# Kernel tuning notes

Measured on AMD Instinct MI355X. Metric: run time of the kernel, lower is better.

The kernel has to match this reference:

```python
import jax, jax.numpy as jnp
import numpy as np

# __init__ constants of RMSELoss(early, gap, late)
EARLY = 1
GAP = 0.5
LATE = 2


def setup_inputs() -> dict:
    key = jax.random.key(0)
    k1, k2 = jax.random.split(key)
    N = 16777216  # rows; column dim is 1 since forward indexes inputs[r, 0]
    inputs = jax.random.normal(k1, (N, 1), dtype=jnp.float32)
    targets = jax.random.normal(k2, (N, 1), dtype=jnp.float32)
    return {"inputs": inputs, "targets": targets}


def reference(inputs, targets):
    # train=True path of RMSELoss.forward, fully vectorized.
    d = targets - inputs  # [N, 1]
    # per-row weight: 2+early if d>=gap, 2+late if d<0, else 0 (d**0 == 1,
    # including 0**0 == 1, matching torch.pow semantics).
    early_term = d ** (2 + EARLY)  # integer_pow handles negative bases exactly
    late_term = d ** (2 + LATE)
    v = jnp.where(d >= GAP, early_term,
                  jnp.where(d < 0, late_term, jnp.ones_like(d)))
    return jnp.mean(v) ** 0.5
```

## Files before the change

### kernel.cpp

```cpp
#include <hip/hip_runtime.h>
#include <math.h>


__device__ __forceinline__ float vfun(float d) {
    float d2 = d * d;
    float e  = d2 * d;
    float l  = d2 * d2;
    return d >= 0.5f ? e : (d < 0.0f ? l : 1.0f);
}

__global__ __launch_bounds__(256) void rmse_partial(
        const float4* __restrict__ x4,
        const float4* __restrict__ t4,
        const float*  __restrict__ x,
        const float*  __restrict__ t,
        float* __restrict__ sum_ws,
        int n4, int n) {
    int idx    = blockIdx.x * blockDim.x + threadIdx.x;
    int stride = gridDim.x * blockDim.x;

    float acc = 0.0f;
    for (int i = idx; i < n4; i += stride) {
        float4 a = x4[i];
        float4 b = t4[i];
        acc += vfun(b.x - a.x);
        acc += vfun(b.y - a.y);
        acc += vfun(b.z - a.z);
        acc += vfun(b.w - a.w);
    }
    if (idx == 0) {
        for (int i = n4 * 4; i < n; ++i) acc += vfun(t[i] - x[i]);
    }

    #pragma unroll
    for (int off = 32; off > 0; off >>= 1)
        acc += __shfl_down(acc, off, 64);

    __shared__ float smem[4];
    int lane = threadIdx.x & 63;
    int wave = threadIdx.x >> 6;
    if (lane == 0) smem[wave] = acc;
    __syncthreads();
    if (threadIdx.x == 0) {
        float s = smem[0] + smem[1] + smem[2] + smem[3];
        atomicAdd(sum_ws, s);
    }
}

__global__ void rmse_final(const float* __restrict__ sum_ws,
                           float* __restrict__ out, float inv_n) {
    out[0] = sqrtf(sum_ws[0] * inv_n);
}

extern "C" void kernel_launch(void* const* d_in, const int* in_sizes, int n_in,
                              void* d_out, int out_size, void* d_ws, size_t ws_size,
                              hipStream_t stream) {
    const float* x = (const float*)d_in[0];
    const float* t = (const float*)d_in[1];
    float* out = (float*)d_out;
    float* ws  = (float*)d_ws;

    int n  = in_sizes[0];
    int n4 = n / 4;

    hipMemsetAsync(ws, 0, sizeof(float), stream);

    int grid = 2048;
    rmse_partial<<<grid, 256, 0, stream>>>(
        (const float4*)x, (const float4*)t, x, t, ws, n4, n);

    rmse_final<<<1, 1, 0, stream>>>(ws, out, 1.0f / (float)n);
}
```

Before: 161.9 us.

## Unroll loads 4x, replace atomics and memset with per-block partials reduction

The main loop now issues four float4 loads per input before computing, which raises memory-level parallelism in this bandwidth-bound reduction. The global atomicAdd and the hipMemsetAsync are removed: each block writes its partial sum to the workspace, and a 256-thread final kernel reduces the 2048 partials. This drops one launch and avoids serialised atomics, at the cost of more live registers and a larger final kernel.

```diff
diff --git a/kernel.cpp b/kernel.cpp
--- a/kernel.cpp
+++ b/kernel.cpp
@@ -1,6 +1,10 @@
 #include <hip/hip_runtime.h>
 #include <math.h>
 
+
+#define BLOCK 256
+#define GRID  2048
+#define NWAVE (BLOCK / 64)
 
 __device__ __forceinline__ float vfun(float d) {
     float d2 = d * d;
@@ -9,47 +13,82 @@
     return d >= 0.5f ? e : (d < 0.0f ? l : 1.0f);
 }
 
-__global__ __launch_bounds__(256) void rmse_partial(
+__device__ __forceinline__ float vfun4(float4 a, float4 b) {
+    return vfun(b.x - a.x) + vfun(b.y - a.y) + vfun(b.z - a.z) + vfun(b.w - a.w);
+}
+
+__global__ __launch_bounds__(BLOCK) void rmse_partial(
         const float4* __restrict__ x4,
         const float4* __restrict__ t4,
         const float*  __restrict__ x,
         const float*  __restrict__ t,
-        float* __restrict__ sum_ws,
+        float* __restrict__ block_sums,
         int n4, int n) {
     int idx    = blockIdx.x * blockDim.x + threadIdx.x;
     int stride = gridDim.x * blockDim.x;
 
     float acc = 0.0f;
-    for (int i = idx; i < n4; i += stride) {
-        float4 a = x4[i];
-        float4 b = t4[i];
-        acc += vfun(b.x - a.x);
-        acc += vfun(b.y - a.y);
-        acc += vfun(b.z - a.z);
-        acc += vfun(b.w - a.w);
+    int i = idx;
+
+    for (; i + 3 * stride < n4; i += 4 * stride) {
+        float4 a0 = x4[i];
+        float4 a1 = x4[i + stride];
+        float4 a2 = x4[i + 2 * stride];
+        float4 a3 = x4[i + 3 * stride];
+        float4 b0 = t4[i];
+        float4 b1 = t4[i + stride];
+        float4 b2 = t4[i + 2 * stride];
+        float4 b3 = t4[i + 3 * stride];
+        acc += vfun4(a0, b0);
+        acc += vfun4(a1, b1);
+        acc += vfun4(a2, b2);
+        acc += vfun4(a3, b3);
+    }
+    for (; i < n4; i += stride) {
+        acc += vfun4(x4[i], t4[i]);
     }
     if (idx == 0) {
-        for (int i = n4 * 4; i < n; ++i) acc += vfun(t[i] - x[i]);
+        for (int j = n4 * 4; j < n; ++j) acc += vfun(t[j] - x[j]);
     }
 
     #pragma unroll
     for (int off = 32; off > 0; off >>= 1)
         acc += __shfl_down(acc, off, 64);
 
-    __shared__ float smem[4];
+    __shared__ float smem[NWAVE];
     int lane = threadIdx.x & 63;
     int wave = threadIdx.x >> 6;
     if (lane == 0) smem[wave] = acc;
     __syncthreads();
     if (threadIdx.x == 0) {
-        float s = smem[0] + smem[1] + smem[2] + smem[3];
-        atomicAdd(sum_ws, s);
+        float s = 0.0f;
+        #pragma unroll
+        for (int w = 0; w < NWAVE; ++w) s += smem[w];
+        block_sums[blockIdx.x] = s;
     }
 }
 
-__global__ void rmse_final(const float* __restrict__ sum_ws,
-                           float* __restrict__ out, float inv_n) {
-    out[0] = sqrtf(sum_ws[0] * inv_n);
+__global__ __launch_bounds__(BLOCK) void rmse_final(
+        const float* __restrict__ block_sums,
+        float* __restrict__ out, float inv_n, int nb) {
+    float s = 0.0f;
+    for (int i = threadIdx.x; i < nb; i += BLOCK) s += block_sums[i];
+
+    #pragma unroll
+    for (int off = 32; off > 0; off >>= 1)
+        s += __shfl_down(s, off, 64);
+
+    __shared__ float smem[NWAVE];
+    int lane = threadIdx.x & 63;
+    int wave = threadIdx.x >> 6;
+    if (lane == 0) smem[wave] = s;
+    __syncthreads();
+    if (threadIdx.x == 0) {
+        float tot = 0.0f;
+        #pragma unroll
+        for (int w = 0; w < NWAVE; ++w) tot += smem[w];
+        out[0] = sqrtf(tot * inv_n);
+    }
 }
 
 extern "C" void kernel_launch(void* const* d_in, const int* in_sizes, int n_in,
@@ -63,11 +102,8 @@
     int n  = in_sizes[0];
     int n4 = n / 4;
 
-    hipMemsetAsync(ws, 0, sizeof(float), stream);
-
-    int grid = 2048;
-    rmse_partial<<<grid, 256, 0, stream>>>(
+    rmse_partial<<<GRID, BLOCK, 0, stream>>>(
         (const float4*)x, (const float4*)t, x, t, ws, n4, n);
 
-    rmse_final<<<1, 1, 0, stream>>>(ws, out, 1.0f / (float)n);
+    rmse_final<<<1, BLOCK, 0, stream>>>(ws, out, 1.0f / (float)n, GRID);
 }
```

After: 144.5 us. 1.12x faster.
